# Kernel optimization log

Measured on AMD Instinct MI355X. Metric: run time of the kernel, lower is better.

Reference implementation:

```python
import jax, jax.numpy as jnp
import numpy as np

N = 100000   # nodes
E = 1200000  # directed edges (avg degree 12)
D = 64       # in_feats
C = 40       # n_classes
K = 16       # propagation steps
ALPHA = 0.05


def setup_inputs() -> dict:
    key = jax.random.key(0)
    k1, k2, k3, k4 = jax.random.split(key, 4)
    feat = jax.random.normal(k1, (N, D), jnp.float32)
    # xavier_uniform for fc.weight [C, D]
    limit = np.sqrt(6.0 / (D + C)).astype(np.float32)
    W = jax.random.uniform(k2, (C, D), jnp.float32, -limit, limit)
    b = jnp.zeros((C,), jnp.float32)
    src = jax.random.randint(k3, (E,), 0, N, dtype=jnp.int32)
    dst = jax.random.randint(k4, (E,), 0, N, dtype=jnp.int32)
    return {"feat": feat, "W": W, "b": b, "src": src, "dst": dst}


def reference(feat, W, b, src, dst):
    # --- getNormAugAdj: A_hat = D^{-1/2} (A + I) D^{-1/2} ---
    loops = jnp.arange(N, dtype=src.dtype)
    row = jnp.concatenate([dst, loops])  # output node of each edge
    col = jnp.concatenate([src, loops])  # input  node of each edge
    ones = jnp.ones(row.shape, feat.dtype)
    deg = jax.ops.segment_sum(ones, row, num_segments=N)  # >= 1 (self-loops)
    dinv = jax.lax.rsqrt(deg)
    w = dinv[row] * dinv[col]  # per-edge normalized weight

    def spmm(x):  # x: [N, D] -> A_hat @ x
        return jax.ops.segment_sum(w[:, None] * x[col], row, num_segments=N)

    feat_ori = feat

    # SSGC loop (faithful to the original, including h /= K inside the loop)
    def step(carry, _):
        x, h = carry
        x = spmm(x)
        h = (h + (1.0 - ALPHA) * x + ALPHA * feat_ori) / K
        return (x, h), None

    (_, h), _ = jax.lax.scan(step, (feat, jnp.zeros_like(feat)), None, length=K)

    # fc(h)
    return h @ W.T + b
```

## Files before the change

kernel.cpp:

```cpp
#include <hip/hip_runtime.h>
#include <hip/hip_fp16.h>

#define NN 100000
#define EE 1200000
#define DD 64
#define CC 40
#define KK 16
#define BSZ 196
#define NBK 512
#define TCAP 3072
#define EPB 4096
#define ABLK ((EE + EPB - 1) / EPB)

#define SLT 261
#define SLT4 196
#define GRID8 (8 * SLT)
#define CH 4096

typedef int   v4i __attribute__((ext_vector_type(4)));
typedef float v4f __attribute__((ext_vector_type(4)));

__device__ __forceinline__ v4i ntld_i4(const int* p) {
    return __builtin_nontemporal_load((const v4i*)p);
}
__device__ __forceinline__ float4 ntld_f4(const float4* p) {
    v4f v = __builtin_nontemporal_load((const v4f*)p);
    return make_float4(v.x, v.y, v.z, v.w);
}
__device__ __forceinline__ void ntst_f4(float4* p, float4 f) {
    v4f v; v.x = f.x; v.y = f.y; v.z = f.z; v.w = f.w;
    __builtin_nontemporal_store(v, (v4f*)p);
}

__global__ __launch_bounds__(512) void curinit_kernel(int* __restrict__ cursor) {
    int b = threadIdx.x;
    if (b < NBK) cursor[b] = b * TCAP;
}

__global__ __launch_bounds__(256) void sortA_kernel(const int* __restrict__ src,
                                                    const int* __restrict__ dst,
                                                    int* __restrict__ cursor,
                                                    int2* __restrict__ tmp) {
    __shared__ int2 stg[EPB];
    __shared__ int hist[NBK], loff[NBK], lcur[NBK], gbase[NBK];
    int t = threadIdx.x;
    long e0 = (long)blockIdx.x * EPB;
    int n = (int)((EE - e0 < EPB) ? (EE - e0) : EPB);
    for (int j = t; j < NBK; j += 256) hist[j] = 0;
    __syncthreads();
    int d[16], sx[16];
#pragma unroll
    for (int j = 0; j < 16; ++j) {
        int i = t + j * 256;
        if (i < n) {
            d[j] = dst[e0 + i];
            sx[j] = src[e0 + i];
            atomicAdd(&hist[d[j] / BSZ], 1);
        } else d[j] = -1;
    }
    __syncthreads();
    int c0 = hist[2 * t], c1 = hist[2 * t + 1];
    int s2 = c0 + c1;
    __syncthreads();
    loff[t] = s2;
    __syncthreads();
    for (int off = 1; off < 256; off <<= 1) {
        int u = (t >= off) ? loff[t - off] : 0;
        __syncthreads();
        loff[t] += u;
        __syncthreads();
    }
    int excl = loff[t] - s2;
    __syncthreads();
    loff[2 * t] = excl;          loff[2 * t + 1] = excl + c0;
    lcur[2 * t] = excl;          lcur[2 * t + 1] = excl + c0;
    gbase[2 * t]     = atomicAdd(&cursor[2 * t], c0);
    gbase[2 * t + 1] = atomicAdd(&cursor[2 * t + 1], c1);
    __syncthreads();
#pragma unroll
    for (int j = 0; j < 16; ++j) {
        if (d[j] >= 0) {
            int b = d[j] / BSZ;
            int p = atomicAdd(&lcur[b], 1);
            stg[p] = make_int2(d[j], sx[j]);
        }
    }
    __syncthreads();
    for (int i = t; i < n; i += 256) {
        int2 r = stg[i];
        int b = r.x / BSZ;
        int pos = gbase[b] + (i - loff[b]);
        if (pos < (b + 1) * TCAP) tmp[pos] = r;
    }
}

__global__ __launch_bounds__(512) void bscan_kernel(const int* __restrict__ cursor,
                                                    int* __restrict__ bbase,
                                                    int* __restrict__ row_ptr) {
    __shared__ int sm[512];
    int t = threadIdx.x;
    int v = (t < NBK) ? (cursor[t] - t * TCAP) : 0;
    sm[t] = v;
    __syncthreads();
    for (int off = 1; off < 512; off <<= 1) {
        int u = (t >= off) ? sm[t - off] : 0;
        __syncthreads();
        sm[t] += u;
        __syncthreads();
    }
    if (t < NBK) bbase[t] = sm[t] - v;
    if (t == 511) row_ptr[NN] = sm[511];
}

__global__ __launch_bounds__(256) void sortB_kernel(const int2* __restrict__ tmp,
                                                    const int* __restrict__ cursor,
                                                    const int* __restrict__ bbase,
                                                    float* __restrict__ dinv,
                                                    float* __restrict__ sqd,
                                                    int* __restrict__ row_ptr,
                                                    int* __restrict__ er_src) {
    __shared__ int2 se[TCAP];
    __shared__ int so[TCAP];
    __shared__ int hist[256], lcur[256];
    int b = blockIdx.x;
    int n0 = b * BSZ;
    if (n0 >= NN) return;
    int n1 = n0 + BSZ; if (n1 > NN) n1 = NN;
    int nb = n1 - n0;
    int t = threadIdx.x;
    int cnt = cursor[b] - b * TCAP;
    int base = bbase[b];
    hist[t] = 0;
    __syncthreads();
    for (int i = t; i < cnt; i += 256) {
        int2 r = tmp[b * TCAP + i];
        se[i] = r;
        atomicAdd(&hist[r.x - n0], 1);
    }
    __syncthreads();
    if (t < nb) {
        float dg = (float)(hist[t] + 1);
        dinv[n0 + t] = rsqrtf(dg);
        sqd[n0 + t]  = sqrtf(dg);
    }
    int v = hist[t];
    lcur[t] = v;
    __syncthreads();
    for (int off = 1; off < 256; off <<= 1) {
        int u = (t >= off) ? lcur[t - off] : 0;
        __syncthreads();
        lcur[t] += u;
        __syncthreads();
    }
    int excl = lcur[t] - v;
    __syncthreads();
    lcur[t] = excl;
    if (t < nb) row_ptr[n0 + t] = base + excl;
    __syncthreads();
    for (int i = t; i < cnt; i += 256) {
        int2 r = se[i];
        int ln = r.x - n0;
        int pos = atomicAdd(&lcur[ln], 1);
        so[pos] = r.y;
    }
    __syncthreads();
    for (int i = t; i < cnt; i += 256) er_src[base + i] = so[i];
}

__global__ __launch_bounds__(256) void proj_kernel(const float4* __restrict__ feat4,
                                                   const float* __restrict__ W,
                                                   const float* __restrict__ dinv,
                                                   float4* __restrict__ z0) {
    __shared__ float smW[CC * 68];
    __shared__ float smF[64 * 68];
    __shared__ float smO[64 * 42];
    int t = threadIdx.x;
    for (int j = t; j < CC * 16; j += 256) {
        int c = j >> 4, q = j & 15;
        *(float4*)(smW + c * 68 + q * 4) = ((const float4*)W)[j];
    }
    int n0 = blockIdx.x * 64;
    for (int j = t; j < 64 * 16; j += 256) {
        int r = j >> 4, q = j & 15;
        if (n0 + r < NN)
            *(float4*)(smF + r * 68 + q * 4) = feat4[(size_t)(n0 + r) * 16 + q];
    }
    __syncthreads();
    int ln = t >> 2, c0 = (t & 3) * 10;
    int node = n0 + ln;
    float acc[10];
#pragma unroll
    for (int c = 0; c < 10; ++c) acc[c] = 0.f;
    if (node < NN) {
#pragma unroll
        for (int db = 0; db < 16; ++db) {
            float4 fv = *(const float4*)(smF + ln * 68 + db * 4);
#pragma unroll
            for (int c = 0; c < 10; ++c) {
                float4 wv = *(const float4*)(smW + (c0 + c) * 68 + db * 4);
                acc[c] = fmaf(fv.x, wv.x, acc[c]);
                acc[c] = fmaf(fv.y, wv.y, acc[c]);
                acc[c] = fmaf(fv.z, wv.z, acc[c]);
                acc[c] = fmaf(fv.w, wv.w, acc[c]);
            }
        }
    }
#pragma unroll
    for (int c = 0; c < 10; ++c) smO[ln * 42 + c0 + c] = acc[c];
    __syncthreads();
    for (int j = t; j < 64 * 5; j += 256) {
        int r = j & 63, q = j >> 6;
        int g = n0 + r;
        if (g < NN) {
            float dv = dinv[g];
            const float* s = smO + r * 42 + q * 8;
            float4 ov;
            __half2* op = (__half2*)&ov;
            op[0] = __floats2half2_rn(dv * s[0], dv * s[1]);
            op[1] = __floats2half2_rn(dv * s[2], dv * s[3]);
            op[2] = __floats2half2_rn(dv * s[4], dv * s[5]);
            op[3] = __floats2half2_rn(dv * s[6], dv * s[7]);
            size_t idx = (q < 2) ? ((size_t)g * 2 + q)
                       : (q < 4) ? ((size_t)2 * NN + (size_t)g * 2 + (q - 2))
                                 : ((size_t)4 * NN + g);
            z0[idx] = ov;
        }
    }
}

#define DEC8(V, F0, F1, F2, F3)                                             \
    const __half2* hp_##F0 = (const __half2*)&(V);                          \
    float2 F0 = __half22float2(hp_##F0[0]), F1 = __half22float2(hp_##F0[1]);\
    float2 F2 = __half22float2(hp_##F0[2]), F3 = __half22float2(hp_##F0[3]);

#define ACC8U(V)                                                            \
    {                                                                       \
        DEC8(V, f0, f1, f2, f3)                                             \
        a0 += f0.x; a1 += f0.y; a2 += f1.x; a3 += f1.y;                     \
        a4 += f2.x; a5 += f2.y; a6 += f3.x; a7 += f3.y;                     \
    }

#define GATHER_WINDOW(XP, STR, PL)                                          \
    {                                                                       \
        int lo = (beg > W0) ? beg : W0;                                     \
        int hi = (end < W1) ? end : W1;                                     \
        int e = lo;                                                         \
        for (; e + 8 <= hi; e += 8) {                                       \
            int s0 = sidx[e - A0 + 0], s1 = sidx[e - A0 + 1];               \
            int s2 = sidx[e - A0 + 2], s3 = sidx[e - A0 + 3];               \
            int s4 = sidx[e - A0 + 4], s5 = sidx[e - A0 + 5];               \
            int s6 = sidx[e - A0 + 6], s7 = sidx[e - A0 + 7];               \
            float4 v0 = (XP)[s0 * (STR) + (PL)];                            \
            float4 v1 = (XP)[s1 * (STR) + (PL)];                            \
            float4 v2 = (XP)[s2 * (STR) + (PL)];                            \
            float4 v3 = (XP)[s3 * (STR) + (PL)];                            \
            float4 v4 = (XP)[s4 * (STR) + (PL)];                            \
            float4 v5 = (XP)[s5 * (STR) + (PL)];                            \
            float4 v6 = (XP)[s6 * (STR) + (PL)];                            \
            float4 v7 = (XP)[s7 * (STR) + (PL)];                            \
            ACC8U(v0); ACC8U(v1); ACC8U(v2); ACC8U(v3);                     \
            ACC8U(v4); ACC8U(v5); ACC8U(v6); ACC8U(v7);                     \
        }                                                                   \
        if (e + 4 <= hi) {                                                  \
            int s0 = sidx[e - A0 + 0], s1 = sidx[e - A0 + 1];               \
            int s2 = sidx[e - A0 + 2], s3 = sidx[e - A0 + 3];               \
            float4 v0 = (XP)[s0 * (STR) + (PL)];                            \
            float4 v1 = (XP)[s1 * (STR) + (PL)];                            \
            float4 v2 = (XP)[s2 * (STR) + (PL)];                            \
            float4 v3 = (XP)[s3 * (STR) + (PL)];                            \
            ACC8U(v0); ACC8U(v1); ACC8U(v2); ACC8U(v3);                     \
            e += 4;                                                         \
        }                                                                   \
        for (; e < hi; ++e) {                                               \
            int s = sidx[e - A0];                                           \
            float4 v = (XP)[s * (STR) + (PL)];                              \
            ACC8U(v);                                                       \
        }                                                                   \
    }

#define STAGE_WINDOW                                                        \
    int W1 = (W0 + CH < blkE) ? (W0 + CH) : blkE;                           \
    int A0 = W0 & ~3;                                                       \
    __syncthreads();                                                        \
    for (int i = A0 + (int)threadIdx.x * 4; i < W1; i += 1024) {            \
        *(v4i*)(sidx + (i - A0)) = ntld_i4(es + i);                         \
    }                                                                       \
    __syncthreads();

template <int STR>
__device__ __forceinline__ void prop_body(
    int* sidx, int n0, int n1, int g, bool act, int pl, size_t off,
    const float4* __restrict__ x, float4* __restrict__ x_out,
    const int* __restrict__ row_ptr, const int* __restrict__ es,
    const float* __restrict__ dinv) {
    const float4* xp = x + off;
    int beg = 0, end = 0, sb = 0;
    float w2 = 0.f;
    float a0 = 0, a1 = 0, a2 = 0, a3 = 0, a4 = 0, a5 = 0, a6 = 0, a7 = 0;
    if (act) {
        beg = row_ptr[g]; end = row_ptr[g + 1];
        float di = dinv[g];
        w2 = di * di;
        sb = g * STR + pl;
        float4 sv = xp[sb];
        DEC8(sv, f0, f1, f2, f3)
        a0 = f0.x; a1 = f0.y; a2 = f1.x; a3 = f1.y;
        a4 = f2.x; a5 = f2.y; a6 = f3.x; a7 = f3.y;
    }
    int blkB = row_ptr[n0], blkE = row_ptr[n1];
    for (int W0 = blkB; W0 < blkE; W0 += CH) {
        STAGE_WINDOW
        if (act) GATHER_WINDOW(xp, STR, pl)
    }
    if (act) {
        float4 ov;
        __half2* op = (__half2*)&ov;
        op[0] = __floats2half2_rn(w2 * a0, w2 * a1);
        op[1] = __floats2half2_rn(w2 * a2, w2 * a3);
        op[2] = __floats2half2_rn(w2 * a4, w2 * a5);
        op[3] = __floats2half2_rn(w2 * a6, w2 * a7);
        ntst_f4(x_out + off + sb, ov);
    }
}

__global__ __launch_bounds__(256) void spmm_prop(
    const float4* __restrict__ x, float4* __restrict__ x_out,
    const int* __restrict__ row_ptr, const int* __restrict__ es,
    const float* __restrict__ dinv) {
    __shared__ __align__(16) int sidx[CH + 8];
    int xcd = blockIdx.x & 7;
    int slot = blockIdx.x >> 3;
    int t = threadIdx.x;
    if (xcd < 6) {
        int part = (xcd < 3) ? xcd : xcd - 3;
        int grp  = (xcd < 3) ? 0 : 1;
        int b0 = (part == 0) ? 0 : ((part == 1) ? 33334 : 66667);
        int b1 = (part == 0) ? 33334 : ((part == 1) ? 66667 : 100000);
        int n0 = b0 + slot * 128;
        int n1 = (n0 + 128 < b1) ? (n0 + 128) : b1;
        int g = n0 + (t >> 1);
        prop_body<2>(sidx, n0, n1, g, g < n1, t & 1, (size_t)grp * 2 * NN,
                     x, x_out, row_ptr, es, dinv);
    } else {
        if (slot >= SLT4) return;
        int b0 = (xcd - 6) * 50000;
        int lim = b0 + 50000;
        int n0 = b0 + slot * 256;
        int n1 = (n0 + 256 < lim) ? (n0 + 256) : lim;
        int g = n0 + t;
        prop_body<1>(sidx, n0, n1, g, g < n1, 0, (size_t)4 * NN,
                     x, x_out, row_ptr, es, dinv);
    }
}

template <int STR>
__device__ __forceinline__ void final_body(
    int* sidx, int n0, int n1, int g, bool act, int pl, int p, size_t off,
    const float4* __restrict__ x15, const float4* __restrict__ x13p,
    const float4* __restrict__ x14p, const float4* __restrict__ z0p,
    const float* __restrict__ bias,
    const int* __restrict__ row_ptr, const int* __restrict__ es,
    const float* __restrict__ dinv, const float* __restrict__ sqd,
    float* __restrict__ outp) {
    const float4* xp = x15 + off;
    int beg = 0, end = 0, sb = 0;
    float di = 0.f, sq = 0.f;
    float s0 = 0, s1 = 0, s2 = 0, s3 = 0, s4 = 0, s5 = 0, s6 = 0, s7 = 0;
    float a0 = 0, a1 = 0, a2 = 0, a3 = 0, a4 = 0, a5 = 0, a6 = 0, a7 = 0;
    if (act) {
        beg = row_ptr[g]; end = row_ptr[g + 1];
        di = dinv[g];
        sq = sqd[g];
        sb = g * STR + pl;
        float4 sv = xp[sb];
        DEC8(sv, f0, f1, f2, f3)
        s0 = f0.x; s1 = f0.y; s2 = f1.x; s3 = f1.y;
        s4 = f2.x; s5 = f2.y; s6 = f3.x; s7 = f3.y;
        a0 = s0; a1 = s1; a2 = s2; a3 = s3;
        a4 = s4; a5 = s5; a6 = s6; a7 = s7;
    }
    int blkB = row_ptr[n0], blkE = row_ptr[n1];
    for (int W0 = blkB; W0 < blkE; W0 += CH) {
        STAGE_WINDOW
        if (act) GATHER_WINDOW(xp, STR, pl)
    }
    if (!act) return;
    size_t gi = off + sb;
    const float C16 = 0.95f / 16.0f;
    const float C15 = 0.95f / 256.0f;
    const float C14 = 0.95f / 4096.0f;
    const float C13 = 0.95f / 65536.0f;
    const float FC  = 0.05f / 15.0f;
    float t0 = C15 * s0, t1 = C15 * s1, t2 = C15 * s2, t3 = C15 * s3;
    float t4 = C15 * s4, t5 = C15 * s5, t6 = C15 * s6, t7 = C15 * s7;
#define ADD8T(P, CF)                                                        \
    {                                                                       \
        float4 v = ntld_f4((P) + gi);                                       \
        DEC8(v, f0, f1, f2, f3)                                             \
        t0 = fmaf((CF), f0.x, t0); t1 = fmaf((CF), f0.y, t1);               \
        t2 = fmaf((CF), f1.x, t2); t3 = fmaf((CF), f1.y, t3);               \
        t4 = fmaf((CF), f2.x, t4); t5 = fmaf((CF), f2.y, t5);               \
        t6 = fmaf((CF), f3.x, t6); t7 = fmaf((CF), f3.y, t7);               \
    }
    ADD8T(x14p, C14)
    ADD8T(x13p, C13)
    ADD8T(z0p, FC)
#undef ADD8T
    float cd = C16 * di;
    float o0 = fmaf(sq, t0, cd * a0), o1 = fmaf(sq, t1, cd * a1);
    float o2 = fmaf(sq, t2, cd * a2), o3 = fmaf(sq, t3, cd * a3);
    float o4 = fmaf(sq, t4, cd * a4), o5 = fmaf(sq, t5, cd * a5);
    float o6 = fmaf(sq, t6, cd * a6), o7 = fmaf(sq, t7, cd * a7);
    const float4* b4 = (const float4*)(bias + p * 8);
    float4 bb0 = b4[0], bb1 = b4[1];
    float4* op = (float4*)(outp + (size_t)g * CC + p * 8);
    ntst_f4(op,     make_float4(o0 + bb0.x, o1 + bb0.y, o2 + bb0.z, o3 + bb0.w));
    ntst_f4(op + 1, make_float4(o4 + bb1.x, o5 + bb1.y, o6 + bb1.z, o7 + bb1.w));
}

__global__ __launch_bounds__(256) void spmm_final(
    const float4* __restrict__ x15, const float4* __restrict__ x13p,
    const float4* __restrict__ x14p, const float4* __restrict__ z0p,
    const float* __restrict__ bias,
    const int* __restrict__ row_ptr, const int* __restrict__ es,
    const float* __restrict__ dinv, const float* __restrict__ sqd,
    float* __restrict__ outp) {
    __shared__ __align__(16) int sidx[CH + 8];
    int xcd = blockIdx.x & 7;
    int slot = blockIdx.x >> 3;
    int t = threadIdx.x;
    if (xcd < 6) {
        int part = (xcd < 3) ? xcd : xcd - 3;
        int grp  = (xcd < 3) ? 0 : 1;
        int b0 = (part == 0) ? 0 : ((part == 1) ? 33334 : 66667);
        int b1 = (part == 0) ? 33334 : ((part == 1) ? 66667 : 100000);
        int n0 = b0 + slot * 128;
        int n1 = (n0 + 128 < b1) ? (n0 + 128) : b1;
        int g = n0 + (t >> 1);
        int pl = t & 1;
        final_body<2>(sidx, n0, n1, g, g < n1, pl, grp * 2 + pl, (size_t)grp * 2 * NN,
                      x15, x13p, x14p, z0p, bias, row_ptr, es, dinv, sqd, outp);
    } else {
        if (slot >= SLT4) return;
        int b0 = (xcd - 6) * 50000;
        int lim = b0 + 50000;
        int n0 = b0 + slot * 256;
        int n1 = (n0 + 256 < lim) ? (n0 + 256) : lim;
        int g = n0 + t;
        final_body<1>(sidx, n0, n1, g, g < n1, 0, 4, (size_t)4 * NN,
                      x15, x13p, x14p, z0p, bias, row_ptr, es, dinv, sqd, outp);
    }
}

extern "C" void kernel_launch(void* const* d_in, const int* in_sizes, int n_in,
                              void* d_out, int out_size, void* d_ws, size_t ws_size,
                              hipStream_t stream) {
    const float* feat = (const float*)d_in[0];
    const float* W    = (const float*)d_in[1];
    const float* b    = (const float*)d_in[2];
    const int*   src  = (const int*)d_in[3];
    const int*   dst  = (const int*)d_in[4];
    float* out = (float*)d_out;

    char* p = (char*)d_ws;
    auto alloc = [&](size_t bytes) {
        char* r = p;
        p += (bytes + 255) & ~(size_t)255;
        return r;
    };
    float*   dinv    = (float*)alloc((size_t)NN * sizeof(float));
    float*   sqd     = (float*)alloc((size_t)NN * sizeof(float));
    int*     row_ptr = (int*)alloc((size_t)(NN + 1) * sizeof(int));
    int*     cursor  = (int*)alloc((size_t)NBK * sizeof(int));
    int*     bbase   = (int*)alloc((size_t)NBK * sizeof(int));
    int2*    tmp     = (int2*)alloc((size_t)NBK * TCAP * sizeof(int2));
    int*     er_src  = (int*)alloc((size_t)EE * sizeof(int) + 64);
    float4*  z0      = (float4*)alloc((size_t)NN * 5 * sizeof(float4));
    float4*  xa      = (float4*)alloc((size_t)NN * 5 * sizeof(float4));
    float4*  xb      = (float4*)alloc((size_t)NN * 5 * sizeof(float4));
    float4*  z13     = (float4*)alloc((size_t)NN * 5 * sizeof(float4));
    float4*  z14     = (float4*)alloc((size_t)NN * 5 * sizeof(float4));
    float4*  z15     = (float4*)alloc((size_t)NN * 5 * sizeof(float4));

    curinit_kernel<<<1, 512, 0, stream>>>(cursor);
    sortA_kernel<<<ABLK, 256, 0, stream>>>(src, dst, cursor, tmp);
    bscan_kernel<<<1, 512, 0, stream>>>(cursor, bbase, row_ptr);
    sortB_kernel<<<NBK, 256, 0, stream>>>(tmp, cursor, bbase, dinv, sqd, row_ptr, er_src);
    proj_kernel<<<(NN + 63) / 64, 256, 0, stream>>>((const float4*)feat, W, dinv, z0);

    const float4* xs = z0;
    for (int j = 0; j < 12; ++j) {
        float4* xd = (j & 1) ? xb : xa;
        spmm_prop<<<GRID8, 256, 0, stream>>>(xs, xd, row_ptr, er_src, dinv);
        xs = xd;
    }
    spmm_prop<<<GRID8, 256, 0, stream>>>(xs, z13, row_ptr, er_src, dinv);
    spmm_prop<<<GRID8, 256, 0, stream>>>(z13, z14, row_ptr, er_src, dinv);
    spmm_prop<<<GRID8, 256, 0, stream>>>(z14, z15, row_ptr, er_src, dinv);
    spmm_final<<<GRID8, 256, 0, stream>>>(z15, z13, z14, z0, b, row_ptr,
                                          er_src, dinv, sqd, out);
}
```

Before: 547.8 us.

## Repartition 40-col feature slabs: one 32-col slab on 4 XCDs, 8-col tail on 4

Changes the fp16 propagated-feature layout from two 16-column interleaved groups plus an 8-column tail into a single 32-column group stored per node (4 float4 chunks) plus the 8-column tail. The spmm and final kernels now map four XCDs to the 32-column slab with 4 lanes per node over quarter-ranges of nodes, and the other four XCDs to the tail slab, instead of a 3+3+2 XCD split. The aim is to balance work across XCDs and to make each gathered neighbor row a contiguous 64-byte fetch, so fewer separate gather passes are needed. The tail XCDs now cover only a quarter of the nodes each, which may leave them underloaded relative to the wide-slab XCDs.

```diff
diff --git a/kernel.cpp b/kernel.cpp
--- a/kernel.cpp
+++ b/kernel.cpp
@@ -5,16 +5,15 @@
 #define EE 1200000
 #define DD 64
 #define CC 40
-#define KK 16
 #define BSZ 196
 #define NBK 512
 #define TCAP 3072
 #define EPB 4096
 #define ABLK ((EE + EPB - 1) / EPB)
 
-#define SLT 261
-#define SLT4 196
-#define GRID8 (8 * SLT)
+#define SL1 391
+#define SL2 98
+#define GRID8 (8 * SL1)
 #define CH 4096
 
 typedef int   v4i __attribute__((ext_vector_type(4)));
@@ -208,8 +207,8 @@
 #pragma unroll
     for (int c = 0; c < 10; ++c) smO[ln * 42 + c0 + c] = acc[c];
     __syncthreads();
-    for (int j = t; j < 64 * 5; j += 256) {
-        int r = j & 63, q = j >> 6;
+    {
+        int r = t >> 2, q = t & 3;
         int g = n0 + r;
         if (g < NN) {
             float dv = dinv[g];
@@ -220,10 +219,21 @@
             op[1] = __floats2half2_rn(dv * s[2], dv * s[3]);
             op[2] = __floats2half2_rn(dv * s[4], dv * s[5]);
             op[3] = __floats2half2_rn(dv * s[6], dv * s[7]);
-            size_t idx = (q < 2) ? ((size_t)g * 2 + q)
-                       : (q < 4) ? ((size_t)2 * NN + (size_t)g * 2 + (q - 2))
-                                 : ((size_t)4 * NN + g);
-            z0[idx] = ov;
+            z0[(size_t)g * 4 + q] = ov;
+        }
+    }
+    if (t < 64) {
+        int g = n0 + t;
+        if (g < NN) {
+            float dv = dinv[g];
+            const float* s = smO + t * 42 + 32;
+            float4 ov;
+            __half2* op = (__half2*)&ov;
+            op[0] = __floats2half2_rn(dv * s[0], dv * s[1]);
+            op[1] = __floats2half2_rn(dv * s[2], dv * s[3]);
+            op[2] = __floats2half2_rn(dv * s[4], dv * s[5]);
+            op[3] = __floats2half2_rn(dv * s[6], dv * s[7]);
+            z0[(size_t)4 * NN + g] = ov;
         }
     }
 }
@@ -331,22 +341,18 @@
     int xcd = blockIdx.x & 7;
     int slot = blockIdx.x >> 3;
     int t = threadIdx.x;
-    if (xcd < 6) {
-        int part = (xcd < 3) ? xcd : xcd - 3;
-        int grp  = (xcd < 3) ? 0 : 1;
-        int b0 = (part == 0) ? 0 : ((part == 1) ? 33334 : 66667);
-        int b1 = (part == 0) ? 33334 : ((part == 1) ? 66667 : 100000);
-        int n0 = b0 + slot * 128;
-        int n1 = (n0 + 128 < b1) ? (n0 + 128) : b1;
-        int g = n0 + (t >> 1);
-        prop_body<2>(sidx, n0, n1, g, g < n1, t & 1, (size_t)grp * 2 * NN,
+    if (xcd < 4) {
+        int q0 = xcd * 25000;
+        int n0 = q0 + slot * 64;
+        int n1 = (n0 + 64 < q0 + 25000) ? (n0 + 64) : (q0 + 25000);
+        int g = n0 + (t >> 2);
+        prop_body<4>(sidx, n0, n1, g, g < n1, t & 3, 0,
                      x, x_out, row_ptr, es, dinv);
     } else {
-        if (slot >= SLT4) return;
-        int b0 = (xcd - 6) * 50000;
-        int lim = b0 + 50000;
-        int n0 = b0 + slot * 256;
-        int n1 = (n0 + 256 < lim) ? (n0 + 256) : lim;
+        if (slot >= SL2) return;
+        int q0 = (xcd - 4) * 25000;
+        int n0 = q0 + slot * 256;
+        int n1 = (n0 + 256 < q0 + 25000) ? (n0 + 256) : (q0 + 25000);
         int g = n0 + t;
         prop_body<1>(sidx, n0, n1, g, g < n1, 0, (size_t)4 * NN,
                      x, x_out, row_ptr, es, dinv);
@@ -429,23 +435,19 @@
     int xcd = blockIdx.x & 7;
     int slot = blockIdx.x >> 3;
     int t = threadIdx.x;
-    if (xcd < 6) {
-        int part = (xcd < 3) ? xcd : xcd - 3;
-        int grp  = (xcd < 3) ? 0 : 1;
-        int b0 = (part == 0) ? 0 : ((part == 1) ? 33334 : 66667);
-        int b1 = (part == 0) ? 33334 : ((part == 1) ? 66667 : 100000);
-        int n0 = b0 + slot * 128;
-        int n1 = (n0 + 128 < b1) ? (n0 + 128) : b1;
-        int g = n0 + (t >> 1);
-        int pl = t & 1;
-        final_body<2>(sidx, n0, n1, g, g < n1, pl, grp * 2 + pl, (size_t)grp * 2 * NN,
+    if (xcd < 4) {
+        int q0 = xcd * 25000;
+        int n0 = q0 + slot * 64;
+        int n1 = (n0 + 64 < q0 + 25000) ? (n0 + 64) : (q0 + 25000);
+        int g = n0 + (t >> 2);
+        int pl = t & 3;
+        final_body<4>(sidx, n0, n1, g, g < n1, pl, pl, 0,
                       x15, x13p, x14p, z0p, bias, row_ptr, es, dinv, sqd, outp);
     } else {
-        if (slot >= SLT4) return;
-        int b0 = (xcd - 6) * 50000;
-        int lim = b0 + 50000;
-        int n0 = b0 + slot * 256;
-        int n1 = (n0 + 256 < lim) ? (n0 + 256) : lim;
+        if (slot >= SL2) return;
+        int q0 = (xcd - 4) * 25000;
+        int n0 = q0 + slot * 256;
+        int n1 = (n0 + 256 < q0 + 25000) ? (n0 + 256) : (q0 + 25000);
         int g = n0 + t;
         final_body<1>(sidx, n0, n1, g, g < n1, 0, 4, (size_t)4 * NN,
                       x15, x13p, x14p, z0p, bias, row_ptr, es, dinv, sqd, outp);
```

New measurement: 519.8 us. 5.1% less time.
